# Kernel optimization log

Measured on AMD Instinct MI355X. Metric: run time of the kernel, lower is better.

Reference implementation:

```python
import jax, jax.numpy as jnp
import numpy as np

E = 8          # num_experts
K = 2          # top_k
R = 16         # lora_r
SCALING = 32.0 / 16.0  # lora_alpha / lora_r

B, S, H, I = 2, 2048, 2048, 8192


def setup_inputs() -> dict:
    key = jax.random.key(0)
    ks = jax.random.split(key, 11)
    inv_h = 1.0 / np.sqrt(H)
    inv_i = 1.0 / np.sqrt(I)
    return {
        "x": jax.random.normal(ks[0], (B, S, H), jnp.float32),
        "gate_W": jax.random.normal(ks[1], (I, H), jnp.float32) * inv_h,
        "up_W": jax.random.normal(ks[2], (I, H), jnp.float32) * inv_h,
        "down_W": jax.random.normal(ks[3], (H, I), jnp.float32) * inv_i,
        "router_W": jax.random.normal(ks[4], (E, H), jnp.float32) * 0.02,
        "gate_A": jax.random.normal(ks[5], (E, R, H), jnp.float32) * inv_h,
        "gate_B": jax.random.normal(ks[6], (E, I, R), jnp.float32) * 0.01,
        "up_A": jax.random.normal(ks[7], (E, R, H), jnp.float32) * inv_h,
        "up_B": jax.random.normal(ks[8], (E, I, R), jnp.float32) * 0.01,
        "down_A": jax.random.normal(ks[9], (E, R, I), jnp.float32) * inv_i,
        "down_B": jax.random.normal(ks[10], (E, H, R), jnp.float32) * 0.01,
    }


def _mixlora_forward(x, gate_W, up_W, down_W, router_W,
                     gate_A, gate_B, up_A, up_B, down_A, down_B):
    b, s, h = x.shape
    T = b * s
    xf = x.reshape(T, h)                                  # [T, H]

    # Shared base FFN projections (computed once for all experts)
    gate_out = xf @ gate_W.T                              # [T, I]
    up_out = xf @ up_W.T                                  # [T, I]

    # Router: softmax in fp32, top-k, renormalize selected weights
    logits = xf @ router_W.T                              # [T, E]
    probs = jax.nn.softmax(logits.astype(jnp.float32), axis=-1)
    w, idx = jax.lax.top_k(probs, K)                      # [T, K]
    w = w / jnp.sum(w, axis=-1, keepdims=True)

    # Dense per-(token, expert) combine weights; 0 for unselected experts
    onehot = jax.nn.one_hot(idx, E, dtype=probs.dtype)    # [T, K, E]
    w_dense = jnp.einsum('tke,tk->te', onehot, w)         # [T, E]

    # Load-balance aux loss: N * sum_i f_i * P_i
    f_i = jnp.sum(onehot, axis=(0, 1)) / T
    p_i = jnp.mean(probs, axis=0)
    aux_loss = E * jnp.dot(f_i, p_i)

    # Scan over experts, accumulating weighted intermediate and down-delta.
    # Since down_proj is linear, sum_k w_k * down(inter_k) = down(sum_k w_k * inter_k).
    def step(carry, p):
        acc_int, acc_dd = carry
        gA, gB, uA, uB, dA, dB, we = p                    # we: [T]
        gd = ((xf @ gA.T) @ gB.T) * SCALING               # [T, I]
        ud = ((xf @ uA.T) @ uB.T) * SCALING               # [T, I]
        inter = jax.nn.silu(gate_out + gd) * (up_out + ud)  # SwiGLU intermediate
        dd = ((inter @ dA.T) @ dB.T) * SCALING            # [T, H]
        we = we.astype(xf.dtype)[:, None]
        return (acc_int + we * inter, acc_dd + we * dd), None

    init = (jnp.zeros((T, gate_W.shape[0]), xf.dtype),
            jnp.zeros((T, h), xf.dtype))
    (acc_int, acc_dd), _ = jax.lax.scan(
        step, init, (gate_A, gate_B, up_A, up_B, down_A, down_B, w_dense.T))

    out = acc_int @ down_W.T + acc_dd                     # [T, H]
    return out.reshape(b, s, h), aux_loss


def reference(x, gate_W, up_W, down_W, router_W,
              gate_A, gate_B, up_A, up_B, down_A, down_B):
    return _mixlora_forward(x, gate_W, up_W, down_W, router_W,
                            gate_A, gate_B, up_A, up_B, down_A, down_B)
```

## Files before the change

### kernel.cpp

```cpp
#include <hip/hip_runtime.h>
#include <stdint.h>
#include <stddef.h>

#define DEVINL __device__ __forceinline__

typedef short sv8 __attribute__((ext_vector_type(8)));
typedef unsigned short usv8 __attribute__((ext_vector_type(8)));
typedef unsigned short usv4 __attribute__((ext_vector_type(4)));
typedef float f32x4 __attribute__((ext_vector_type(4)));

constexpr int T_TOK = 4096;
constexpr int H_DIM = 2048;
constexpr int I_DIM = 8192;
constexpr int E_NUM = 8;
constexpr int R_LORA = 16;
constexpr float SCALING = 2.0f;
constexpr int NQ = 4;
constexpr int TQ = T_TOK / NQ;
constexpr int PQ = TQ * 2;
constexpr int P_TOT = T_TOK * 2;

DEVINL float bf2f(unsigned short u) {
  union { uint32_t i; float f; } v; v.i = ((uint32_t)u) << 16; return v.f;
}
DEVINL unsigned short f2bf(float x) {
  union { float f; uint32_t i; } v; v.f = x;
  uint32_t r = v.i + 0x7FFFu + ((v.i >> 16) & 1u);
  return (unsigned short)(r >> 16);
}
DEVINL float bflo(uint32_t w) {
  union { uint32_t i; float f; } v; v.i = w << 16; return v.f;
}
DEVINL float bfhi(uint32_t w) {
  union { uint32_t i; float f; } v; v.i = w & 0xFFFF0000u; return v.f;
}

DEVINL f32x4 MFMA_BF16(sv8 a, sv8 b, f32x4 c) {
  return __builtin_amdgcn_mfma_f32_16x16x32_bf16(a, b, c, 0, 0, 0);
}

DEVINL void load16_to_lds(const void* g, void* l) {
  __builtin_amdgcn_global_load_lds(
      (const __attribute__((address_space(1))) uint32_t*)g,
      (__attribute__((address_space(3))) uint32_t*)l, 16, 0, 0);
}

__global__ void cast_f32_to_bf16(const float4* __restrict__ src, usv4* __restrict__ dst) {
  long i = (long)blockIdx.x * blockDim.x + threadIdx.x;
  float4 v = src[i];
  usv4 o;
  o[0] = f2bf(v.x); o[1] = f2bf(v.y); o[2] = f2bf(v.z); o[3] = f2bf(v.w);
  dst[i] = o;
}

__global__ void zero_lcnt(int* lcnt) {
  if (threadIdx.x < E_NUM * NQ) lcnt[threadIdx.x] = 0;
}

__global__ void router_kernel(const float* __restrict__ x, const float* __restrict__ rW,
                              float* __restrict__ wbuf, int* __restrict__ idxb,
                              float* __restrict__ probs, int* __restrict__ lcnt,
                              int* __restrict__ lists, unsigned short* __restrict__ xf_bf) {
  const int wave = threadIdx.x >> 6, lane = threadIdx.x & 63;
  const int t = blockIdx.x * 4 + wave;
  const float* xr = x + (long)t * H_DIM;
  unsigned short* xbr = xf_bf + (long)t * H_DIM;
  float acc[E_NUM];
#pragma unroll
  for (int e = 0; e < E_NUM; ++e) acc[e] = 0.f;
  for (int h = lane; h < H_DIM; h += 64) {
    float xv = xr[h];
    xbr[h] = f2bf(xv);
#pragma unroll
    for (int e = 0; e < E_NUM; ++e) acc[e] += xv * rW[e * H_DIM + h];
  }
#pragma unroll
  for (int e = 0; e < E_NUM; ++e) {
#pragma unroll
    for (int off = 32; off; off >>= 1) acc[e] += __shfl_xor(acc[e], off);
  }
  if (lane == 0) {
    float mx = acc[0];
#pragma unroll
    for (int e = 1; e < E_NUM; ++e) mx = fmaxf(mx, acc[e]);
    float p[E_NUM];
    float s = 0.f;
#pragma unroll
    for (int e = 0; e < E_NUM; ++e) { p[e] = expf(acc[e] - mx); s += p[e]; }
    float inv = 1.f / s;
#pragma unroll
    for (int e = 0; e < E_NUM; ++e) p[e] *= inv;
    int e1 = 0;
    for (int e = 1; e < E_NUM; ++e) if (p[e] > p[e1]) e1 = e;
    int e2 = (e1 == 0) ? 1 : 0;
    for (int e = 0; e < E_NUM; ++e) if (e != e1 && p[e] > p[e2]) e2 = e;
    float w1 = p[e1], w2 = p[e2], wsum = w1 + w2;
    wbuf[t * 2 + 0] = w1 / wsum;
    wbuf[t * 2 + 1] = w2 / wsum;
    idxb[t * 2 + 0] = e1;
    idxb[t * 2 + 1] = e2;
#pragma unroll
    for (int e = 0; e < E_NUM; ++e) probs[(long)t * E_NUM + e] = p[e];
    const int q = t / TQ;
    int p1 = atomicAdd(&lcnt[e1 * NQ + q], 1); lists[(e1 * NQ + q) * TQ + p1] = t * 2 + 0;
    int p2 = atomicAdd(&lcnt[e2 * NQ + q], 1); lists[(e2 * NQ + q) * TQ + p2] = t * 2 + 1;
  }
}

__global__ void aux_kernel(const float* __restrict__ probs, const int* __restrict__ lcnt,
                           float* __restrict__ aux_out) {
  const int lane = threadIdx.x;
  float s[E_NUM];
#pragma unroll
  for (int e = 0; e < E_NUM; ++e) s[e] = 0.f;
  for (int t = lane; t < T_TOK; t += 64) {
#pragma unroll
    for (int e = 0; e < E_NUM; ++e) s[e] += probs[(long)t * E_NUM + e];
  }
#pragma unroll
  for (int e = 0; e < E_NUM; ++e) {
#pragma unroll
    for (int off = 32; off; off >>= 1) s[e] += __shfl_xor(s[e], off);
  }
  if (lane == 0) {
    float a = 0.f;
#pragma unroll
    for (int e = 0; e < E_NUM; ++e) {
      int cnt = 0;
#pragma unroll
      for (int q = 0; q < NQ; ++q) cnt += lcnt[e * NQ + q];
      a += ((float)cnt / (float)T_TOK) * (s[e] / (float)T_TOK);
    }
    *aux_out = (float)E_NUM * a;
  }
}

__global__ __launch_bounds__(256)
void lora_a_mfma_kernel(const unsigned short* __restrict__ xf_bf,
                        const unsigned short* __restrict__ gA_bf,
                        const unsigned short* __restrict__ uA_bf,
                        const int* __restrict__ lists, const int* __restrict__ lcnt,
                        float* __restrict__ vg, float* __restrict__ vu) {
  const int q = blockIdx.x / (E_NUM * 16);
  const int rem = blockIdx.x % (E_NUM * 16);
  const int e = rem >> 4;
  const int wave = threadIdx.x >> 6, lane = threadIdx.x & 63;
  const int grp = (rem & 15) * 4 + wave;
  const int npairs = lcnt[e * NQ + q];
  if (grp * 16 >= npairs) return;
  const int* lst = lists + (e * NQ + q) * TQ;
  const int slot = lane & 15;
  int pidx = grp * 16 + slot;
  int pair = lst[(pidx < npairs) ? pidx : grp * 16];
  int t = pair >> 1;
  const long kb = (long)blockIdx.y * 1024 + (lane >> 4) * 8;
  const unsigned short* arow = xf_bf + (long)t * H_DIM + kb;
  const unsigned short* bg = gA_bf + ((long)e * R_LORA + slot) * H_DIM + kb;
  const unsigned short* bu = uA_bf + ((long)e * R_LORA + slot) * H_DIM + kb;
  f32x4 ag = {}, au = {};
#pragma unroll 4
  for (int k = 0; k < 1024; k += 32) {
    sv8 a = *(const sv8*)(arow + k);
    ag = MFMA_BF16(a, *(const sv8*)(bg + k), ag);
    au = MFMA_BF16(a, *(const sv8*)(bu + k), au);
  }
  const int orow = (lane >> 4) * 4;
  const long base = (long)blockIdx.y * P_TOT;
#pragma unroll
  for (int rg = 0; rg < 4; ++rg) {
    int pidx2 = grp * 16 + orow + rg;
    if (pidx2 < npairs) {
      int pr = lst[pidx2];
      vg[(base + pr) * R_LORA + slot] = ag[rg];
      vu[(base + pr) * R_LORA + slot] = au[rg];
    }
  }
}

__global__ void reduce_uguu_kernel(const float* __restrict__ vg, const float* __restrict__ vu,
                                   float* __restrict__ ug, float* __restrict__ uu) {
  long i = (long)blockIdx.x * 256 + threadIdx.x;
  ug[i] = vg[i] + vg[(long)P_TOT * R_LORA + i];
  uu[i] = vu[i] + vu[(long)P_TOT * R_LORA + i];
}

__global__ __launch_bounds__(256, 2)
void gemm1_kernel(const unsigned short* __restrict__ A,
                  const unsigned short* __restrict__ B0,
                  const unsigned short* __restrict__ B1,
                  unsigned short* __restrict__ C0,
                  unsigned short* __restrict__ C1) {
  constexpr int Kd = H_DIM;
  __shared__ unsigned short As[128 * 32];
  __shared__ unsigned short Bs0[128 * 32];
  __shared__ unsigned short Bs1[128 * 32];
  const int tid = threadIdx.x;
  const int wave = tid >> 6, lane = tid & 63;
  const int wm = wave >> 1, wn = wave & 1;
  int bid = blockIdx.y * gridDim.x + blockIdx.x;
  const int cpx = (gridDim.x * gridDim.y) >> 3;
  bid = (bid & 7) * cpx + (bid >> 3);
  const int bx = bid % gridDim.x, by = bid / gridDim.x;
  const long m0 = (long)by * 128;
  const long n0 = (long)bx * 128;
  f32x4 accG[4][4] = {}, accU[4][4] = {};
  const int srow = wave * 32 + (lane >> 2);
  const int scol = (lane & 3) * 8;
  const unsigned short* Ag  = A  + (m0 + srow) * Kd + scol;
  const unsigned short* B0g = B0 + (n0 + srow) * Kd + scol;
  const unsigned short* B1g = B1 + (n0 + srow) * Kd + scol;
  const int frA = wm * 64 + (lane & 15);
  const int frB = wn * 64 + (lane & 15);
  const int fc = (lane >> 4) * 8;

  for (int k0 = 0; k0 < Kd; k0 += 32) {
    __syncthreads();
#pragma unroll
    for (int c = 0; c < 2; ++c) {
      load16_to_lds(Ag  + (long)c * 16 * Kd + k0, &As [(wave * 32 + c * 16) * 32]);
      load16_to_lds(B0g + (long)c * 16 * Kd + k0, &Bs0[(wave * 32 + c * 16) * 32]);
      load16_to_lds(B1g + (long)c * 16 * Kd + k0, &Bs1[(wave * 32 + c * 16) * 32]);
    }
    __syncthreads();
    sv8 af[4], b0f[4], b1f[4];
#pragma unroll
    for (int m = 0; m < 4; ++m) af[m] = *(const sv8*)&As[(frA + m * 16) * 32 + fc];
#pragma unroll
    for (int n = 0; n < 4; ++n) {
      b0f[n] = *(const sv8*)&Bs0[(frB + n * 16) * 32 + fc];
      b1f[n] = *(const sv8*)&Bs1[(frB + n * 16) * 32 + fc];
    }
#pragma unroll
    for (int m = 0; m < 4; ++m)
#pragma unroll
      for (int n = 0; n < 4; ++n) {
        accG[m][n] = MFMA_BF16(af[m], b0f[n], accG[m][n]);
        accU[m][n] = MFMA_BF16(af[m], b1f[n], accU[m][n]);
      }
  }
  const int rb = (lane >> 4) * 4, cb = lane & 15;
#pragma unroll
  for (int m = 0; m < 4; ++m)
#pragma unroll
    for (int n = 0; n < 4; ++n) {
      long col = n0 + wn * 64 + n * 16 + cb;
#pragma unroll
      for (int r = 0; r < 4; ++r) {
        long row = m0 + wm * 64 + m * 16 + rb + r;
        C0[row * I_DIM + col] = f2bf(accG[m][n][r]);
        C1[row * I_DIM + col] = f2bf(accU[m][n][r]);
      }
    }
}

__global__ __launch_bounds__(256)
void combine2_kernel(const unsigned short* __restrict__ g_bf,
                     const unsigned short* __restrict__ u_bf,
                     const float* __restrict__ gB, const float* __restrict__ uB,
                     const float* __restrict__ ug, const float* __restrict__ uu,
                     const float* __restrict__ wbuf,
                     const int* __restrict__ lists, const int* __restrict__ lcnt,
                     unsigned short* __restrict__ winter, int q) {
  const int e = blockIdx.y >> 4, chunk = blockIdx.y & 15;
  const int npairs = lcnt[e * NQ + q];
  const int pbase = chunk * 64;
  if (pbase >= npairs) return;
  const int wave = threadIdx.x >> 6, lane = threadIdx.x & 63;
  const long i0 = (long)blockIdx.x * 256 + lane * 4;
  uint32_t gbp[32], ubp[32];
#pragma unroll
  for (int j = 0; j < 4; ++j) {
    const float4* gp = (const float4*)(gB + ((long)e * I_DIM + i0 + j) * R_LORA);
    const float4* up = (const float4*)(uB + ((long)e * I_DIM + i0 + j) * R_LORA);
#pragma unroll
    for (int c = 0; c < 4; ++c) {
      float4 gv = gp[c], uv = up[c];
      gbp[j * 8 + c * 2 + 0] = (uint32_t)f2bf(gv.x) | ((uint32_t)f2bf(gv.y) << 16);
      gbp[j * 8 + c * 2 + 1] = (uint32_t)f2bf(gv.z) | ((uint32_t)f2bf(gv.w) << 16);
      ubp[j * 8 + c * 2 + 0] = (uint32_t)f2bf(uv.x) | ((uint32_t)f2bf(uv.y) << 16);
      ubp[j * 8 + c * 2 + 1] = (uint32_t)f2bf(uv.z) | ((uint32_t)f2bf(uv.w) << 16);
    }
  }
  for (int pl = 0; pl < 16; ++pl) {
    int pi = pbase + wave + pl * 4;
    if (pi >= npairs) break;
    int pair = lists[(e * NQ + q) * TQ + pi];
    int t = pair >> 1, plocal = pair - q * PQ;
    float w = wbuf[pair];
    const float2* ug2 = (const float2*)(ug + (long)pair * R_LORA);
    const float2* uu2 = (const float2*)(uu + (long)pair * R_LORA);
    usv4 gv = *(const usv4*)(g_bf + (long)t * I_DIM + i0);
    usv4 uv = *(const usv4*)(u_bf + (long)t * I_DIM + i0);
    float gd[4] = {0.f, 0.f, 0.f, 0.f}, ud[4] = {0.f, 0.f, 0.f, 0.f};
#pragma unroll
    for (int c = 0; c < 8; ++c) {
      float2 a = ug2[c], b = uu2[c];
#pragma unroll
      for (int j = 0; j < 4; ++j) {
        uint32_t gw = gbp[j * 8 + c], uw = ubp[j * 8 + c];
        gd[j] += a.x * bflo(gw) + a.y * bfhi(gw);
        ud[j] += b.x * bflo(uw) + b.y * bfhi(uw);
      }
    }
    usv4 o;
#pragma unroll
    for (int j = 0; j < 4; ++j) {
      float zg = bf2f(gv[j]) + SCALING * gd[j];
      float zu = bf2f(uv[j]) + SCALING * ud[j];
      float sil = zg / (1.f + __expf(-zg));
      o[j] = f2bf(w * sil * zu);
    }
    *(usv4*)(winter + (long)plocal * I_DIM + i0) = o;
  }
}

__global__ void acc_kernel(const unsigned short* __restrict__ winter,
                           unsigned short* __restrict__ acc_bf, int q) {
  long gid = (long)blockIdx.x * 256 + threadIdx.x;
  int tl = (int)(gid >> 10);
  int ig = (int)(gid & 1023);
  int t = q * TQ + tl;
  usv8 a = *(const usv8*)(winter + ((long)(tl * 2 + 0)) * I_DIM + ig * 8);
  usv8 b = *(const usv8*)(winter + ((long)(tl * 2 + 1)) * I_DIM + ig * 8);
  usv8 o;
#pragma unroll
  for (int j = 0; j < 8; ++j) o[j] = f2bf(bf2f(a[j]) + bf2f(b[j]));
  *(usv8*)(acc_bf + (long)t * I_DIM + ig * 8) = o;
}

__global__ __launch_bounds__(256)
void lorav_mfma_kernel(const unsigned short* __restrict__ winter,
                       const unsigned short* __restrict__ dA_bf,
                       const int* __restrict__ lists, const int* __restrict__ lcnt,
                       float* __restrict__ vv, int q) {
  const int e = blockIdx.x >> 4;
  const int wave = threadIdx.x >> 6, lane = threadIdx.x & 63;
  const int grp = (blockIdx.x & 15) * 4 + wave;
  const int npairs = lcnt[e * NQ + q];
  if (grp * 16 >= npairs) return;
  const int* lst = lists + (e * NQ + q) * TQ;
  const int slot = lane & 15;
  int pidx = grp * 16 + slot;
  int pair = lst[(pidx < npairs) ? pidx : grp * 16];
  int plocal = pair - q * PQ;
  const long kb = (long)blockIdx.y * 1024 + (lane >> 4) * 8;
  const unsigned short* arow = winter + (long)plocal * I_DIM + kb;
  const unsigned short* brow = dA_bf + ((long)e * R_LORA + slot) * I_DIM + kb;
  f32x4 acc = {};
#pragma unroll 4
  for (int k = 0; k < 1024; k += 32)
    acc = MFMA_BF16(*(const sv8*)(arow + k), *(const sv8*)(brow + k), acc);
  const int orow = (lane >> 4) * 4;
  const long base = (long)blockIdx.y * P_TOT;
#pragma unroll
  for (int rg = 0; rg < 4; ++rg) {
    int pidx2 = grp * 16 + orow + rg;
    if (pidx2 < npairs) {
      int pr = lst[pidx2];
      vv[(base + pr) * R_LORA + slot] = acc[rg];
    }
  }
}

__global__ void reduce_v_kernel(const float* __restrict__ vv, float* __restrict__ vbuf) {
  long i = (long)blockIdx.x * 256 + threadIdx.x;
  float s = 0.f;
#pragma unroll
  for (int kc = 0; kc < 8; ++kc) s += vv[(long)kc * P_TOT * R_LORA + i];
  vbuf[i] = s;
}

__global__ void dd_kernel(const float* __restrict__ vbuf, const int* __restrict__ idxb,
                          const float* __restrict__ dB,
                          float* __restrict__ out) {
  const int t = blockIdx.y;
  const int h = blockIdx.x * 256 + threadIdx.x;
  const int e0 = idxb[t * 2 + 0], e1 = idxb[t * 2 + 1];
  const float4* v0p = (const float4*)(vbuf + (long)(t * 2 + 0) * R_LORA);
  const float4* v1p = (const float4*)(vbuf + (long)(t * 2 + 1) * R_LORA);
  const float4* b0 = (const float4*)(dB + ((long)e0 * H_DIM + h) * R_LORA);
  const float4* b1 = (const float4*)(dB + ((long)e1 * H_DIM + h) * R_LORA);
  float dd = 0.f;
#pragma unroll
  for (int qq = 0; qq < 4; ++qq) {
    float4 v0 = v0p[qq], x0 = b0[qq];
    float4 v1 = v1p[qq], x1 = b1[qq];
    dd += v0.x * x0.x + v0.y * x0.y + v0.z * x0.z + v0.w * x0.w;
    dd += v1.x * x1.x + v1.y * x1.y + v1.z * x1.z + v1.w * x1.w;
  }
  out[(long)t * H_DIM + h] = SCALING * dd;
}

__global__ __launch_bounds__(256, 2)
void gemm2_kernel(const unsigned short* __restrict__ A,
                  const unsigned short* __restrict__ B,
                  float* __restrict__ out) {
  constexpr int Kd = I_DIM;
  __shared__ unsigned short As[128 * 32];
  __shared__ unsigned short Bs[128 * 32];
  const int tid = threadIdx.x;
  const int wave = tid >> 6, lane = tid & 63;
  const int wm = wave >> 1, wn = wave & 1;
  int bid = blockIdx.y * gridDim.x + blockIdx.x;
  const int cpx = (gridDim.x * gridDim.y) >> 3;
  bid = (bid & 7) * cpx + (bid >> 3);
  const int bx = bid % gridDim.x, by = bid / gridDim.x;
  const long m0 = (long)by * 128;
  const long n0 = (long)bx * 128;
  f32x4 acc[4][4] = {};
  const int srow = wave * 32 + (lane >> 2);
  const int scol = (lane & 3) * 8;
  const unsigned short* Ag = A + (m0 + srow) * Kd + scol;
  const unsigned short* Bg = B + (n0 + srow) * Kd + scol;
  const int frA = wm * 64 + (lane & 15);
  const int frB = wn * 64 + (lane & 15);
  const int fc = (lane >> 4) * 8;

  for (int k0 = 0; k0 < Kd; k0 += 32) {
    __syncthreads();
#pragma unroll
    for (int c = 0; c < 2; ++c) {
      load16_to_lds(Ag + (long)c * 16 * Kd + k0, &As[(wave * 32 + c * 16) * 32]);
      load16_to_lds(Bg + (long)c * 16 * Kd + k0, &Bs[(wave * 32 + c * 16) * 32]);
    }
    __syncthreads();
    sv8 af[4], bf[4];
#pragma unroll
    for (int m = 0; m < 4; ++m) af[m] = *(const sv8*)&As[(frA + m * 16) * 32 + fc];
#pragma unroll
    for (int n = 0; n < 4; ++n) bf[n] = *(const sv8*)&Bs[(frB + n * 16) * 32 + fc];
#pragma unroll
    for (int m = 0; m < 4; ++m)
#pragma unroll
      for (int n = 0; n < 4; ++n) acc[m][n] = MFMA_BF16(af[m], bf[n], acc[m][n]);
  }

  const int rb = (lane >> 4) * 4, cb = lane & 15;
#pragma unroll
  for (int m = 0; m < 4; ++m)
#pragma unroll
    for (int n = 0; n < 4; ++n) {
      long col = n0 + wn * 64 + n * 16 + cb;
#pragma unroll
      for (int r = 0; r < 4; ++r) {
        long row = m0 + wm * 64 + m * 16 + rb + r;
        out[row * H_DIM + col] += acc[m][n][r];
      }
    }
}

extern "C" void kernel_launch(void* const* d_in, const int* in_sizes, int n_in,
                              void* d_out, int out_size, void* d_ws, size_t ws_size,
                              hipStream_t stream) {
  (void)in_sizes; (void)n_in; (void)out_size;
  const float* x        = (const float*)d_in[0];
  const float* gate_W   = (const float*)d_in[1];
  const float* up_W     = (const float*)d_in[2];
  const float* down_W   = (const float*)d_in[3];
  const float* router_W = (const float*)d_in[4];
  const float* gate_A   = (const float*)d_in[5];
  const float* gate_B   = (const float*)d_in[6];
  const float* up_A     = (const float*)d_in[7];
  const float* up_B     = (const float*)d_in[8];
  const float* down_A   = (const float*)d_in[9];
  const float* down_B   = (const float*)d_in[10];
  float* out = (float*)d_out;

  char* ws = (char*)d_ws;
  size_t off = 0;
  auto take = [&](size_t bytes) -> char* {
    char* p = ws + off;
    off += (bytes + 255) & ~(size_t)255;
    return p;
  };
  unsigned short* xf_bf  = (unsigned short*)take((size_t)T_TOK * H_DIM * 2);
  unsigned short* gW_bf  = (unsigned short*)take((size_t)I_DIM * H_DIM * 2);
  unsigned short* uW_bf  = (unsigned short*)take((size_t)I_DIM * H_DIM * 2);
  unsigned short* dA_bf  = (unsigned short*)take((size_t)E_NUM * R_LORA * I_DIM * 2);
  unsigned short* g_bf   = (unsigned short*)take((size_t)T_TOK * I_DIM * 2);
  unsigned short* u_bf   = (unsigned short*)take((size_t)T_TOK * I_DIM * 2);
  unsigned short* winterQ= (unsigned short*)take((size_t)PQ * I_DIM * 2);
  float* wbuf  = (float*)take((size_t)P_TOT * 4);
  int*   idxb  = (int*)take((size_t)P_TOT * 4);
  float* ug    = (float*)take((size_t)P_TOT * R_LORA * 4);
  float* uu    = (float*)take((size_t)P_TOT * R_LORA * 4);
  float* vbuf  = (float*)take((size_t)P_TOT * R_LORA * 4);
  float* probs = (float*)take((size_t)T_TOK * E_NUM * 4);
  int*   lcnt  = (int*)take((size_t)E_NUM * NQ * 4);
  int*   lists = (int*)take((size_t)E_NUM * NQ * TQ * 4);

  unsigned short* dW_bf  = gW_bf;
  unsigned short* acc_bf = g_bf;
  float* vg = (float*)winterQ;
  float* vu = (float*)(winterQ + (size_t)1 * 1024 * 1024 / 2);
  unsigned short* gA_bf = winterQ + (size_t)2 * 1024 * 1024 / 2;
  unsigned short* uA_bf = winterQ + (size_t)5 * 512 * 1024 / 2;
  float* vv = (float*)xf_bf;

  if (ws_size < off) return;

  zero_lcnt<<<1, 64, 0, stream>>>(lcnt);
  router_kernel<<<T_TOK / 4, 256, 0, stream>>>(x, router_W, wbuf, idxb, probs, lcnt, lists, xf_bf);
  aux_kernel<<<1, 64, 0, stream>>>(probs, lcnt, out + (size_t)T_TOK * H_DIM);

  cast_f32_to_bf16<<<(E_NUM * R_LORA * H_DIM / 4) / 256, 256, 0, stream>>>((const float4*)gate_A, (usv4*)gA_bf);
  cast_f32_to_bf16<<<(E_NUM * R_LORA * H_DIM / 4) / 256, 256, 0, stream>>>((const float4*)up_A, (usv4*)uA_bf);
  lora_a_mfma_kernel<<<dim3(NQ * E_NUM * 16, 2), 256, 0, stream>>>(xf_bf, gA_bf, uA_bf, lists, lcnt, vg, vu);
  reduce_uguu_kernel<<<(P_TOT * R_LORA) / 256, 256, 0, stream>>>(vg, vu, ug, uu);

  cast_f32_to_bf16<<<(I_DIM * H_DIM / 4) / 256, 256, 0, stream>>>((const float4*)gate_W, (usv4*)gW_bf);
  cast_f32_to_bf16<<<(I_DIM * H_DIM / 4) / 256, 256, 0, stream>>>((const float4*)up_W, (usv4*)uW_bf);
  cast_f32_to_bf16<<<(E_NUM * R_LORA * I_DIM / 4) / 256, 256, 0, stream>>>((const float4*)down_A, (usv4*)dA_bf);

  gemm1_kernel<<<dim3(I_DIM / 128, T_TOK / 128), 256, 0, stream>>>(xf_bf, gW_bf, uW_bf, g_bf, u_bf);

  cast_f32_to_bf16<<<(H_DIM * I_DIM / 4) / 256, 256, 0, stream>>>((const float4*)down_W, (usv4*)dW_bf);

  for (int q = 0; q < NQ; ++q) {
    combine2_kernel<<<dim3(I_DIM / 256, E_NUM * 16), 256, 0, stream>>>(
        g_bf, u_bf, gate_B, up_B, ug, uu, wbuf, lists, lcnt, winterQ, q);
    acc_kernel<<<(TQ * (I_DIM / 8)) / 256, 256, 0, stream>>>(winterQ, acc_bf, q);
    lorav_mfma_kernel<<<dim3(E_NUM * 16, 8), 256, 0, stream>>>(winterQ, dA_bf, lists, lcnt, vv, q);
  }
  reduce_v_kernel<<<(P_TOT * R_LORA) / 256, 256, 0, stream>>>(vv, vbuf);

  dd_kernel<<<dim3(H_DIM / 256, T_TOK), 256, 0, stream>>>(vbuf, idxb, down_B, out);
  gemm2_kernel<<<dim3(H_DIM / 128, T_TOK / 128), 256, 0, stream>>>(acc_bf, dW_bf, out);
}
```

Baseline: 1.230 ms.

## Replace gemm1 with 256x256 double-buffered 8-wave pipelined GEMM

Replaces the fused gate/up 128x128 GEMM with a 256x256-tile, 512-thread kernel. It splits gate and up into separate grid z-slices, uses 128KB of double-buffered LDS with XOR swizzling, and interleaves staged global-to-LDS loads with MFMA quadrants under barriers and setprio. It also drops the block-index swizzle from gemm2. The aim is to hide memory latency and raise MFMA utilisation, at the cost of losing the shared A-tile reuse across the two weight matrices and putting more pressure on occupancy.

```diff
diff --git a/kernel.cpp b/kernel.cpp
--- a/kernel.cpp
+++ b/kernel.cpp
@@ -44,6 +44,10 @@
       (const __attribute__((address_space(1))) uint32_t*)g,
       (__attribute__((address_space(3))) uint32_t*)l, 16, 0, 0);
 }
+
+#define BARRIER() __builtin_amdgcn_s_barrier()
+#define SB0() __builtin_amdgcn_sched_barrier(0)
+#define LGKM0() asm volatile("s_waitcnt lgkmcnt(0)" ::: "memory")
 
 __global__ void cast_f32_to_bf16(const float4* __restrict__ src, usv4* __restrict__ dst) {
   long i = (long)blockIdx.x * blockDim.x + threadIdx.x;
@@ -184,71 +188,158 @@
   uu[i] = vu[i] + vu[(long)P_TOT * R_LORA + i];
 }
 
-__global__ __launch_bounds__(256, 2)
-void gemm1_kernel(const unsigned short* __restrict__ A,
-                  const unsigned short* __restrict__ B0,
-                  const unsigned short* __restrict__ B1,
-                  unsigned short* __restrict__ C0,
-                  unsigned short* __restrict__ C1) {
-  constexpr int Kd = H_DIM;
-  __shared__ unsigned short As[128 * 32];
-  __shared__ unsigned short Bs0[128 * 32];
-  __shared__ unsigned short Bs1[128 * 32];
+__global__ __launch_bounds__(512, 2)
+void gemm8p_kernel(const unsigned short* __restrict__ A,
+                   const unsigned short* __restrict__ B0,
+                   const unsigned short* __restrict__ B1,
+                   unsigned short* __restrict__ C0,
+                   unsigned short* __restrict__ C1,
+                   int K, int ldc) {
+  extern __shared__ unsigned short lds[];
+  const unsigned short* __restrict__ B = blockIdx.z ? B1 : B0;
+  unsigned short* __restrict__ C = blockIdx.z ? C1 : C0;
   const int tid = threadIdx.x;
   const int wave = tid >> 6, lane = tid & 63;
-  const int wm = wave >> 1, wn = wave & 1;
-  int bid = blockIdx.y * gridDim.x + blockIdx.x;
-  const int cpx = (gridDim.x * gridDim.y) >> 3;
-  bid = (bid & 7) * cpx + (bid >> 3);
-  const int bx = bid % gridDim.x, by = bid / gridDim.x;
-  const long m0 = (long)by * 128;
-  const long n0 = (long)bx * 128;
-  f32x4 accG[4][4] = {}, accU[4][4] = {};
-  const int srow = wave * 32 + (lane >> 2);
-  const int scol = (lane & 3) * 8;
-  const unsigned short* Ag  = A  + (m0 + srow) * Kd + scol;
-  const unsigned short* B0g = B0 + (n0 + srow) * Kd + scol;
-  const unsigned short* B1g = B1 + (n0 + srow) * Kd + scol;
-  const int frA = wm * 64 + (lane & 15);
-  const int frB = wn * 64 + (lane & 15);
-  const int fc = (lane >> 4) * 8;
-
-  for (int k0 = 0; k0 < Kd; k0 += 32) {
-    __syncthreads();
-#pragma unroll
-    for (int c = 0; c < 2; ++c) {
-      load16_to_lds(Ag  + (long)c * 16 * Kd + k0, &As [(wave * 32 + c * 16) * 32]);
-      load16_to_lds(B0g + (long)c * 16 * Kd + k0, &Bs0[(wave * 32 + c * 16) * 32]);
-      load16_to_lds(B1g + (long)c * 16 * Kd + k0, &Bs1[(wave * 32 + c * 16) * 32]);
-    }
-    __syncthreads();
-    sv8 af[4], b0f[4], b1f[4];
-#pragma unroll
-    for (int m = 0; m < 4; ++m) af[m] = *(const sv8*)&As[(frA + m * 16) * 32 + fc];
-#pragma unroll
-    for (int n = 0; n < 4; ++n) {
-      b0f[n] = *(const sv8*)&Bs0[(frB + n * 16) * 32 + fc];
-      b1f[n] = *(const sv8*)&Bs1[(frB + n * 16) * 32 + fc];
-    }
-#pragma unroll
-    for (int m = 0; m < 4; ++m)
-#pragma unroll
-      for (int n = 0; n < 4; ++n) {
-        accG[m][n] = MFMA_BF16(af[m], b0f[n], accG[m][n]);
-        accU[m][n] = MFMA_BF16(af[m], b1f[n], accU[m][n]);
-      }
-  }
+  const int wm = wave >> 2, wn = wave & 3;
+  const long m0 = (long)blockIdx.y * 256;
+  const long n0 = (long)blockIdx.x * 256;
+  const int NT = K >> 6;
+
+  const int lr = lane & 15;
+  const int lc = (lane >> 4) * 8;
+  const int xm = ((lane & 4) << 3) | ((lane & 2) << 3) | ((lane & 1) << 6);
+  const int srow = tid >> 3;
+  const int scol = (tid & 7) * 8;
+  const int gcol = scol ^ (((tid >> 5) & 1) << 4) ^ (((tid >> 4) & 1) << 3)
+                        ^ (((tid >> 3) & 1) << 5);
+
+  f32x4 acc[8][4] = {};
+  sv8 aF[4][2], bF[4][2];
+
+  auto ldsAt = [&](int buf, int mat) -> unsigned short* {
+    return lds + (((buf << 1) + mat) << 14);
+  };
+  auto stageA = [&](int buf, int R, long k0) {
+    load16_to_lds(A + (m0 + R + srow) * K + k0 + gcol,
+                  ldsAt(buf, 0) + ((R + srow) << 6) + scol);
+  };
+  auto stageB = [&](int buf, int R, long k0) {
+    load16_to_lds(B + (n0 + R + srow) * K + k0 + gcol,
+                  ldsAt(buf, 1) + ((R + srow) << 6) + scol);
+  };
+  auto rdA = [&](int buf, int row16, int ks) -> sv8 {
+    int bo = ((((row16 + lr) << 7) + ((ks * 32 + lc) << 1))) ^ xm;
+    return *(const sv8*)((const char*)ldsAt(buf, 0) + bo);
+  };
+  auto rdB = [&](int buf, int row16, int ks) -> sv8 {
+    int bo = ((((row16 + lr) << 7) + ((ks * 32 + lc) << 1))) ^ xm;
+    return *(const sv8*)((const char*)ldsAt(buf, 1) + bo);
+  };
+
+  stageA(0, 0, 0); stageA(0, 64, 0); stageA(0, 128, 0); stageA(0, 192, 0);
+  stageB(0, 0, 0); stageB(0, 64, 0); stageB(0, 128, 0); stageB(0, 192, 0);
+  if (NT > 1) {
+    stageA(1, 0, 64); stageA(1, 128, 64);
+    asm volatile("s_waitcnt vmcnt(2)" ::: "memory");
+  } else {
+    asm volatile("s_waitcnt vmcnt(0)" ::: "memory");
+  }
+  BARRIER();
+
+  for (int t = 0; t < NT; ++t) {
+    const int P = t & 1, Q = P ^ 1;
+    const long kQ = ((long)t + 1) << 6;
+    const long kP2 = ((long)t + 2) << 6;
+    const bool hQ = (t + 1) < NT, hP2 = (t + 2) < NT;
+
+#pragma unroll
+    for (int mf = 0; mf < 4; ++mf)
+#pragma unroll
+      for (int ks = 0; ks < 2; ++ks)
+        aF[mf][ks] = rdA(P, wm * 128 + mf * 16, ks);
+#pragma unroll
+    for (int nf = 0; nf < 2; ++nf)
+#pragma unroll
+      for (int ks = 0; ks < 2; ++ks)
+        bF[nf][ks] = rdB(P, wn * 64 + nf * 16, ks);
+    if (hQ) { stageA(Q, 64, kQ); stageA(Q, 192, kQ); }
+    BARRIER(); LGKM0(); SB0();
+    __builtin_amdgcn_s_setprio(1);
+#pragma unroll
+    for (int mf = 0; mf < 4; ++mf)
+#pragma unroll
+      for (int nf = 0; nf < 2; ++nf)
+#pragma unroll
+        for (int ks = 0; ks < 2; ++ks)
+          acc[mf][nf] = MFMA_BF16(aF[mf][ks], bF[nf][ks], acc[mf][nf]);
+    __builtin_amdgcn_s_setprio(0);
+    BARRIER();
+
+#pragma unroll
+    for (int nf = 0; nf < 2; ++nf)
+#pragma unroll
+      for (int ks = 0; ks < 2; ++ks)
+        bF[2 + nf][ks] = rdB(P, wn * 64 + (2 + nf) * 16, ks);
+    if (hQ) { stageB(Q, 0, kQ); stageB(Q, 64, kQ); }
+    BARRIER(); LGKM0(); SB0();
+    __builtin_amdgcn_s_setprio(1);
+#pragma unroll
+    for (int mf = 0; mf < 4; ++mf)
+#pragma unroll
+      for (int nf = 0; nf < 2; ++nf)
+#pragma unroll
+        for (int ks = 0; ks < 2; ++ks)
+          acc[mf][2 + nf] = MFMA_BF16(aF[mf][ks], bF[2 + nf][ks], acc[mf][2 + nf]);
+    __builtin_amdgcn_s_setprio(0);
+    BARRIER();
+
+#pragma unroll
+    for (int mf = 0; mf < 4; ++mf)
+#pragma unroll
+      for (int ks = 0; ks < 2; ++ks)
+        aF[mf][ks] = rdA(P, wm * 128 + 64 + mf * 16, ks);
+    if (hQ) { stageB(Q, 128, kQ); stageB(Q, 192, kQ); }
+    BARRIER(); LGKM0(); SB0();
+    __builtin_amdgcn_s_setprio(1);
+#pragma unroll
+    for (int mf = 0; mf < 4; ++mf)
+#pragma unroll
+      for (int nf = 0; nf < 2; ++nf)
+#pragma unroll
+        for (int ks = 0; ks < 2; ++ks)
+          acc[4 + mf][nf] = MFMA_BF16(aF[mf][ks], bF[nf][ks], acc[4 + mf][nf]);
+    __builtin_amdgcn_s_setprio(0);
+    BARRIER();
+
+    if (hP2) {
+      stageA(P, 0, kP2); stageA(P, 128, kP2);
+      asm volatile("s_waitcnt vmcnt(2)" ::: "memory");
+    } else {
+      asm volatile("s_waitcnt vmcnt(0)" ::: "memory");
+    }
+    BARRIER(); LGKM0(); SB0();
+    __builtin_amdgcn_s_setprio(1);
+#pragma unroll
+    for (int mf = 0; mf < 4; ++mf)
+#pragma unroll
+      for (int nf = 0; nf < 2; ++nf)
+#pragma unroll
+        for (int ks = 0; ks < 2; ++ks)
+          acc[4 + mf][2 + nf] = MFMA_BF16(aF[mf][ks], bF[2 + nf][ks], acc[4 + mf][2 + nf]);
+    __builtin_amdgcn_s_setprio(0);
+    BARRIER();
+  }
+
   const int rb = (lane >> 4) * 4, cb = lane & 15;
 #pragma unroll
-  for (int m = 0; m < 4; ++m)
-#pragma unroll
-    for (int n = 0; n < 4; ++n) {
-      long col = n0 + wn * 64 + n * 16 + cb;
+  for (int mf = 0; mf < 8; ++mf)
+#pragma unroll
+    for (int nf = 0; nf < 4; ++nf) {
+      long col = n0 + wn * 64 + nf * 16 + cb;
 #pragma unroll
       for (int r = 0; r < 4; ++r) {
-        long row = m0 + wm * 64 + m * 16 + rb + r;
-        C0[row * I_DIM + col] = f2bf(accG[m][n][r]);
-        C1[row * I_DIM + col] = f2bf(accU[m][n][r]);
+        long row = m0 + wm * 128 + mf * 16 + rb + r;
+        C[row * ldc + col] = f2bf(acc[mf][nf][r]);
       }
     }
 }
@@ -401,12 +492,8 @@
   const int tid = threadIdx.x;
   const int wave = tid >> 6, lane = tid & 63;
   const int wm = wave >> 1, wn = wave & 1;
-  int bid = blockIdx.y * gridDim.x + blockIdx.x;
-  const int cpx = (gridDim.x * gridDim.y) >> 3;
-  bid = (bid & 7) * cpx + (bid >> 3);
-  const int bx = bid % gridDim.x, by = bid / gridDim.x;
-  const long m0 = (long)by * 128;
-  const long n0 = (long)bx * 128;
+  const long m0 = (long)blockIdx.y * 128;
+  const long n0 = (long)blockIdx.x * 128;
   f32x4 acc[4][4] = {};
   const int srow = wave * 32 + (lane >> 2);
   const int scol = (lane & 3) * 8;
@@ -512,7 +599,10 @@
   cast_f32_to_bf16<<<(I_DIM * H_DIM / 4) / 256, 256, 0, stream>>>((const float4*)up_W, (usv4*)uW_bf);
   cast_f32_to_bf16<<<(E_NUM * R_LORA * I_DIM / 4) / 256, 256, 0, stream>>>((const float4*)down_A, (usv4*)dA_bf);
 
-  gemm1_kernel<<<dim3(I_DIM / 128, T_TOK / 128), 256, 0, stream>>>(xf_bf, gW_bf, uW_bf, g_bf, u_bf);
+  hipFuncSetAttribute((const void*)gemm8p_kernel,
+                      hipFuncAttributeMaxDynamicSharedMemorySize, 131072);
+  gemm8p_kernel<<<dim3(I_DIM / 256, T_TOK / 256, 2), 512, 131072, stream>>>(
+      xf_bf, gW_bf, uW_bf, g_bf, u_bf, H_DIM, I_DIM);
 
   cast_f32_to_bf16<<<(H_DIM * I_DIM / 4) / 256, 256, 0, stream>>>((const float4*)down_W, (usv4*)dW_bf);
 
```

Result: faster. 1.176 ms (-4.4%).
